# Kernel tuning notes

Measured on AMD Instinct MI355X. Metric: run time of the kernel, lower is better.

Reference implementation:

```python
import jax, jax.numpy as jnp
import numpy as np

DG, UF, Z, FD = 32, 4, 16, 16      # decoder grid, upsample factor, z bins, feat dim
H = W = DG * UF                     # 128 BEV resolution
S = 128                             # depth samples per ray
MLP_H = 32
X_MIN, X_MAX = -51.2, 51.2
Y_MIN, Y_MAX = -51.2, 51.2
Z_MIN, Z_MAX = -5.0, 3.0
D_MIN, D_MAX = 1.0, 50.0


def setup_inputs() -> dict:
    key = jax.random.key(0)
    ks = jax.random.split(key, 8)
    B, R, D = 2, 8192, 512
    out_dim = UF * UF * Z * FD
    s1 = 1.0 / np.sqrt(D); s2 = 1.0 / np.sqrt(FD); s3 = 1.0 / np.sqrt(MLP_H)
    return {
        'decoder_output': jax.random.normal(ks[0], (B, DG * DG, D), jnp.float32),
        'ray_origins': jax.random.normal(ks[1], (B, R, 3), jnp.float32),
        'ray_directions': jax.random.normal(ks[2], (B, R, 3), jnp.float32),
        'ln_g': jnp.ones((D,), jnp.float32),
        'ln_b': jnp.zeros((D,), jnp.float32),
        'W1': jax.random.uniform(ks[3], (D, out_dim), jnp.float32, -s1, s1),
        'b1': jnp.zeros((out_dim,), jnp.float32),
        'W2': jax.random.uniform(ks[4], (FD, MLP_H), jnp.float32, -s2, s2),
        'b2': jnp.zeros((MLP_H,), jnp.float32),
        'W3': jax.random.uniform(ks[5], (MLP_H, 1), jnp.float32, -s3, s3),
        'b3': jnp.zeros((1,), jnp.float32),
    }


def _build_nfg(dec, ln_g, ln_b, W1, b1):
    B = dec.shape[0]
    mu = dec.mean(-1, keepdims=True)
    var = dec.var(-1, keepdims=True)  # biased, matches torch LayerNorm
    x = (dec - mu) / jnp.sqrt(var + 1e-5) * ln_g + ln_b
    x = x @ W1 + b1
    x = x.reshape(B, DG, DG, UF, UF, Z, FD).transpose(0, 1, 3, 2, 4, 5, 6)
    x = x.reshape(B, H, W, Z, FD)
    return x.transpose(0, 4, 3, 1, 2)  # (B, F, Z, H, W)


def _trilinear_one(nfg_b, cw, ch, cd):
    # nfg_b: (F, Z, H, W); cw/ch/cd: (P,) in [-1,1] indexing W/H/Z resp.
    # align_corners=True mapping, zeros padding (mask OOB corners).
    fw = (cw + 1.0) * 0.5 * (W - 1)
    fh = (ch + 1.0) * 0.5 * (H - 1)
    fd = (cd + 1.0) * 0.5 * (Z - 1)
    w0 = jnp.floor(fw); h0 = jnp.floor(fh); d0 = jnp.floor(fd)
    tw = fw - w0; th = fh - h0; td = fd - d0
    out = jnp.zeros((nfg_b.shape[0], cw.shape[0]), nfg_b.dtype)
    for dd in (0, 1):
        for hh in (0, 1):
            for ww in (0, 1):
                di = d0 + dd; hi = h0 + hh; wi = w0 + ww
                wt = ((td if dd else 1.0 - td) * (th if hh else 1.0 - th)
                      * (tw if ww else 1.0 - tw))
                valid = ((di >= 0) & (di <= Z - 1) & (hi >= 0) & (hi <= H - 1)
                         & (wi >= 0) & (wi <= W - 1))
                dic = jnp.clip(di, 0, Z - 1).astype(jnp.int32)
                hic = jnp.clip(hi, 0, H - 1).astype(jnp.int32)
                wic = jnp.clip(wi, 0, W - 1).astype(jnp.int32)
                out = out + nfg_b[:, dic, hic, wic] * (wt * valid)
    return out  # (F, P)


def reference(decoder_output, ray_origins, ray_directions,
              ln_g, ln_b, W1, b1, W2, b2, W3, b3):
    nfg = _build_nfg(decoder_output, ln_g, ln_b, W1, b1)  # (B,F,Z,H,W)
    B, R, _ = ray_origins.shape
    t = jnp.linspace(0.0, 1.0, S, dtype=jnp.float32)
    depths = D_MIN + (D_MAX - D_MIN) * t                       # (S,)
    pts = ray_origins[:, :, None, :] + ray_directions[:, :, None, :] * depths[None, None, :, None]
    xn = 2.0 * (pts[..., 0] - X_MIN) / (X_MAX - X_MIN) - 1.0
    yn = 2.0 * (pts[..., 1] - Y_MIN) / (Y_MAX - Y_MIN) - 1.0
    zn = 2.0 * (pts[..., 2] - Z_MIN) / (Z_MAX - Z_MIN) - 1.0
    # torch grid_sample grid last dim = (x,y,z) -> (W,H,D); grid was stacked [y,x,z]
    cw = yn.reshape(B, -1); ch = xn.reshape(B, -1); cd = zn.reshape(B, -1)
    feats = jax.vmap(_trilinear_one)(nfg, cw, ch, cd)          # (B, F, R*S)
    feats = feats.transpose(0, 2, 1).reshape(B, R, S, FD)
    h = jax.nn.relu(feats @ W2 + b2)
    alpha = jax.nn.sigmoid((h @ W3 + b3)[..., 0])              # (B, R, S)
    oma = 1.0 - alpha + 1e-10
    trans = jnp.cumprod(
        jnp.concatenate([jnp.ones((B, R, 1), alpha.dtype), oma[..., :-1]], -1), -1)
    weights = alpha * trans
    pred_depths = (weights * depths[None, None, :]).sum(-1)    # (B, R)
    return pred_depths, weights, nfg
```

## Files before the change

### kernel.cpp

```cpp
#include <hip/hip_runtime.h>
#include <math.h>

#define DG   32
#define UF   4
#define ZB   16
#define FD   16
#define HH   128
#define WWID 128
#define SNUM 128
#define BATCH 2
#define RAYS  8192
#define NTOK  2048
#define DINP  512
#define ODIM  4096
#define MLPH  32

#define OUT_PRED_OFF 0
#define OUT_W_OFF    (BATCH*RAYS)
#define OUT_NFG_OFF  (OUT_W_OFF + BATCH*RAYS*SNUM)

typedef _Float16 half8 __attribute__((ext_vector_type(8)));
typedef _Float16 half4 __attribute__((ext_vector_type(4)));
typedef _Float16 h2 __attribute__((ext_vector_type(2)));
typedef float f32x4 __attribute__((ext_vector_type(4)));

#define GLDS16(gp, lp) \
    __builtin_amdgcn_global_load_lds((const __attribute__((address_space(1))) void*)(gp), \
                                     (__attribute__((address_space(3))) void*)(lp), 16, 0, 0)

__global__ __launch_bounds__(256) void ln_kernel(const float* __restrict__ dec,
                                                 const float* __restrict__ lng,
                                                 const float* __restrict__ lnb,
                                                 const float* __restrict__ W2,
                                                 const float* __restrict__ b2,
                                                 const float* __restrict__ W3,
                                                 _Float16* __restrict__ Af,
                                                 _Float16* __restrict__ W2f,
                                                 float* __restrict__ b2f,
                                                 float* __restrict__ w3f) {
    int t = blockIdx.x;
    int tid = threadIdx.x;
    const float2* row = reinterpret_cast<const float2*>(dec + (size_t)t * DINP);
    float2 v = row[tid];

    __shared__ float red[4];
    __shared__ float stat[2];

    float s = v.x + v.y;
    #pragma unroll
    for (int o = 32; o > 0; o >>= 1) s += __shfl_down(s, o);
    if ((tid & 63) == 0) red[tid >> 6] = s;
    __syncthreads();
    if (tid == 0) stat[0] = (red[0] + red[1] + red[2] + red[3]) * (1.0f / DINP);
    __syncthreads();
    float mu = stat[0];

    float dx = v.x - mu, dy = v.y - mu;
    float q = dx * dx + dy * dy;
    #pragma unroll
    for (int o = 32; o > 0; o >>= 1) q += __shfl_down(q, o);
    if ((tid & 63) == 0) red[tid >> 6] = q;
    __syncthreads();
    if (tid == 0) {
        float var = (red[0] + red[1] + red[2] + red[3]) * (1.0f / DINP);
        stat[1] = 1.0f / sqrtf(var + 1e-5f);
    }
    __syncthreads();
    float rstd = stat[1];

    int c = 2 * tid;
    h2 o2;
    o2.x = (_Float16)(dx * rstd * lng[c]     + lnb[c]);
    o2.y = (_Float16)(dy * rstd * lng[c + 1] + lnb[c + 1]);
    *reinterpret_cast<h2*>(Af + (size_t)t * DINP + c) = o2;

    if (blockIdx.x == 0 && tid < 128) {
        int jt = tid >> 6, l = tid & 63;
        int sub = l & 15, g = l >> 4;
        #pragma unroll
        for (int e = 0; e < 4; ++e) {
            W2f[(jt * 64 + l) * 4 + e] = (_Float16)W2[(g * 4 + e) * MLPH + jt * 16 + sub];
            b2f[(jt * 64 + l) * 4 + e] = b2[jt * 16 + g * 4 + e];
            w3f[(jt * 64 + l) * 4 + e] = W3[jt * 16 + g * 4 + e];
        }
    }
}

__global__ __launch_bounds__(256) void w1prep_kernel(const float* __restrict__ W1,
                                                     _Float16* __restrict__ W1T) {
    __shared__ float st[64][65];
    int c0 = blockIdx.x * 64;
    int k0 = blockIdx.y * 64;
    int tid = threadIdx.x;
    {
        int r = tid >> 2, cq = (tid & 3) * 16;
        const float* src = W1 + (size_t)(k0 + r) * ODIM + c0 + cq;
        #pragma unroll
        for (int q = 0; q < 4; ++q) {
            float4 v = *reinterpret_cast<const float4*>(src + q * 4);
            st[r][cq + q * 4 + 0] = v.x;
            st[r][cq + q * 4 + 1] = v.y;
            st[r][cq + q * 4 + 2] = v.z;
            st[r][cq + q * 4 + 3] = v.w;
        }
    }
    __syncthreads();
    {
        int cc = tid >> 2, kq = (tid & 3) * 16;
        _Float16 tmp[16];
        #pragma unroll
        for (int i = 0; i < 16; ++i) tmp[i] = (_Float16)st[kq + i][cc];
        _Float16* dst = W1T + (size_t)(c0 + cc) * DINP + k0 + kq;
        *reinterpret_cast<half8*>(dst)     = *reinterpret_cast<half8*>(&tmp[0]);
        *reinterpret_cast<half8*>(dst + 8) = *reinterpret_cast<half8*>(&tmp[8]);
    }
}

__global__ __launch_bounds__(256, 2) void gemm_mfma_kernel(
        const _Float16* __restrict__ Af, const _Float16* __restrict__ W1T,
        const float* __restrict__ bias, _Float16* __restrict__ gh) {
    __shared__ _Float16 As[128 * 32];
    __shared__ _Float16 Bs[128 * 32];

    int tid = threadIdx.x;
    int l = tid & 63, w = tid >> 6;
    int wr = w >> 1, wc = w & 1;
    int row0 = blockIdx.y * 128;
    int col0 = blockIdx.x * 128;

    const char* Ag0 = (const char*)Af + (size_t)(row0 + w * 32 + (l >> 2)) * (DINP * 2) + (l & 3) * 16;
    const char* Ag1 = Ag0 + 16 * (DINP * 2);
    const char* Bg0 = (const char*)W1T + (size_t)(col0 + w * 32 + (l >> 2)) * (DINP * 2) + (l & 3) * 16;
    const char* Bg1 = Bg0 + 16 * (DINP * 2);
    char* lA0 = (char*)As + w * 2048;
    char* lA1 = lA0 + 1024;
    char* lB0 = (char*)Bs + w * 2048;
    char* lB1 = lB0 + 1024;

    f32x4 acc[4][4] = {};

    for (int kk = 0; kk < DINP; kk += 32) {
        GLDS16(Ag0, lA0); GLDS16(Ag1, lA1);
        GLDS16(Bg0, lB0); GLDS16(Bg1, lB1);
        Ag0 += 64; Ag1 += 64; Bg0 += 64; Bg1 += 64;
        __syncthreads();

        half8 af[4], bf[4];
        #pragma unroll
        for (int m = 0; m < 4; ++m)
            af[m] = *reinterpret_cast<const half8*>(As + (wr * 64 + m * 16 + (l & 15)) * 32 + (l >> 4) * 8);
        #pragma unroll
        for (int n = 0; n < 4; ++n)
            bf[n] = *reinterpret_cast<const half8*>(Bs + (wc * 64 + n * 16 + (l & 15)) * 32 + (l >> 4) * 8);
        #pragma unroll
        for (int m = 0; m < 4; ++m)
            #pragma unroll
            for (int n = 0; n < 4; ++n)
                acc[m][n] = __builtin_amdgcn_mfma_f32_16x16x32_f16(af[m], bf[n], acc[m][n], 0, 0, 0);
        __syncthreads();
    }

    #pragma unroll
    for (int n = 0; n < 4; ++n) {
        int c = col0 + wc * 64 + n * 16 + (l & 15);
        float bv = bias[c];
        int f = c & 15, z = (c >> 4) & 15, v = (c >> 8) & 3, u = (c >> 10) & 3;
        #pragma unroll
        for (int m = 0; m < 4; ++m) {
            int rbase = row0 + wr * 64 + m * 16 + ((l >> 4) << 2);
            #pragma unroll
            for (int j = 0; j < 4; ++j) {
                int t = rbase + j;
                int bb = t >> 10;
                int g = t & 1023;
                int i = g >> 5, j2 = g & 31;
                int h = i * 4 + u, wq = j2 * 4 + v;
                size_t gaddr = ((((size_t)(bb * ZB + z) * HH + h) * WWID + wq) << 4) + f;
                gh[gaddr] = (_Float16)(acc[m][n][j] + bv);
            }
        }
    }
}

__global__ __launch_bounds__(256) void tp_kernel(const _Float16* __restrict__ gh,
                                                 float* __restrict__ nfg) {
    int blk = blockIdx.x;
    int bb = blk >> 11, z = (blk >> 7) & 15, h = blk & 127;
    __shared__ float sl[128 * 17];
    int tid = threadIdx.x;
    const uint4* src = reinterpret_cast<const uint4*>(gh + (size_t)blk * 2048);
    uint4 v = src[tid];
    int wv = tid >> 1, fb = (tid & 1) * 8;
    h2 p0 = __builtin_bit_cast(h2, v.x);
    h2 p1 = __builtin_bit_cast(h2, v.y);
    h2 p2 = __builtin_bit_cast(h2, v.z);
    h2 p3 = __builtin_bit_cast(h2, v.w);
    float* sr = &sl[wv * 17 + fb];
    sr[0] = (float)p0.x; sr[1] = (float)p0.y;
    sr[2] = (float)p1.x; sr[3] = (float)p1.y;
    sr[4] = (float)p2.x; sr[5] = (float)p2.y;
    sr[6] = (float)p3.x; sr[7] = (float)p3.y;
    __syncthreads();
    int f = tid >> 4, w0 = (tid & 15) * 8;
    float* dst = nfg + (((size_t)(bb * FD + f) * ZB + z) * (HH * WWID)) + h * WWID + w0;
    float4 o0, o1;
    o0.x = sl[(w0 + 0) * 17 + f]; o0.y = sl[(w0 + 1) * 17 + f];
    o0.z = sl[(w0 + 2) * 17 + f]; o0.w = sl[(w0 + 3) * 17 + f];
    o1.x = sl[(w0 + 4) * 17 + f]; o1.y = sl[(w0 + 5) * 17 + f];
    o1.z = sl[(w0 + 6) * 17 + f]; o1.w = sl[(w0 + 7) * 17 + f];
    *reinterpret_cast<float4*>(dst) = o0;
    *reinterpret_cast<float4*>(dst + 4) = o1;
}

__device__ __forceinline__ void gather_feat(const _Float16* __restrict__ gb,
                                            float px, float py, float pz,
                                            h2* __restrict__ a) {
    float fw = (py * (1.0f / 51.2f) + 1.0f) * 63.5f;
    float fh = (px * (1.0f / 51.2f) + 1.0f) * 63.5f;
    float fd = (pz + 5.0f) * (0.25f * 7.5f);
    float w0f = floorf(fw), h0f = floorf(fh), d0f = floorf(fd);
    float tw = fw - w0f, th = fh - h0f, td = fd - d0f;
    int w0 = (int)w0f, h0 = (int)h0f, d0 = (int)d0f;

    float aw0 = (w0 >= 0 && w0 <= WWID - 1) ? (1.0f - tw) : 0.0f;
    float aw1 = (w0 + 1 >= 0 && w0 + 1 <= WWID - 1) ? tw : 0.0f;
    float ah0 = (h0 >= 0 && h0 <= HH - 1) ? (1.0f - th) : 0.0f;
    float ah1 = (h0 + 1 >= 0 && h0 + 1 <= HH - 1) ? th : 0.0f;
    float ad0 = (d0 >= 0 && d0 <= ZB - 1) ? (1.0f - td) : 0.0f;
    float ad1 = (d0 + 1 >= 0 && d0 + 1 <= ZB - 1) ? td : 0.0f;

    if ((ad0 + ad1) * (ah0 + ah1) * (aw0 + aw1) <= 0.0f) return;

    int w0c = min(max(w0, 0), WWID - 1), w1c = min(max(w0 + 1, 0), WWID - 1);
    int h0c = min(max(h0, 0), HH - 1),   h1c = min(max(h0 + 1, 0), HH - 1);
    int d0c = min(max(d0, 0), ZB - 1),   d1c = min(max(d0 + 1, 0), ZB - 1);

    int od0 = d0c * (HH * WWID * FD), od1 = d1c * (HH * WWID * FD);
    int oh0 = h0c * (WWID * FD),      oh1 = h1c * (WWID * FD);
    int ow0 = w0c * FD,               ow1 = w1c * FD;

#define CORNER(OFF, WF) do { \
        const uint4* cp_ = reinterpret_cast<const uint4*>(gb + (OFF)); \
        uint4 A_ = cp_[0], B_ = cp_[1]; \
        _Float16 wh_ = (_Float16)(WF); \
        h2 w2_ = {wh_, wh_}; \
        a[0] += __builtin_bit_cast(h2, A_.x) * w2_; \
        a[1] += __builtin_bit_cast(h2, A_.y) * w2_; \
        a[2] += __builtin_bit_cast(h2, A_.z) * w2_; \
        a[3] += __builtin_bit_cast(h2, A_.w) * w2_; \
        a[4] += __builtin_bit_cast(h2, B_.x) * w2_; \
        a[5] += __builtin_bit_cast(h2, B_.y) * w2_; \
        a[6] += __builtin_bit_cast(h2, B_.z) * w2_; \
        a[7] += __builtin_bit_cast(h2, B_.w) * w2_; \
    } while (0)

    CORNER(od0 + oh0 + ow0, ad0 * ah0 * aw0);
    CORNER(od0 + oh0 + ow1, ad0 * ah0 * aw1);
    CORNER(od0 + oh1 + ow0, ad0 * ah1 * aw0);
    CORNER(od0 + oh1 + ow1, ad0 * ah1 * aw1);
    CORNER(od1 + oh0 + ow0, ad1 * ah0 * aw0);
    CORNER(od1 + oh0 + ow1, ad1 * ah0 * aw1);
    CORNER(od1 + oh1 + ow0, ad1 * ah1 * aw0);
    CORNER(od1 + oh1 + ow1, ad1 * ah1 * aw1);
#undef CORNER
}

#define SF 24
__global__ __launch_bounds__(256) void ray_fused_kernel(
        const float* __restrict__ orig, const float* __restrict__ dirs,
        const _Float16* __restrict__ gh,
        const _Float16* __restrict__ W2f, const float* __restrict__ b2f,
        const float* __restrict__ w3f, const float* __restrict__ b3,
        float* __restrict__ pred_out, float* __restrict__ w_out) {
    int tid = threadIdx.x;
    int lane = tid & 63, wvid = tid >> 6;
    int ray = blockIdx.x * 4 + wvid;
    int bb = ray >> 13;

    __shared__ _Float16 featLDS[4 * 128 * SF];
    _Float16* FL = &featLDS[wvid * 128 * SF];

    const float* o3 = orig + (size_t)ray * 3;
    const float* d3 = dirs + (size_t)ray * 3;
    float ox = o3[0], oy = o3[1], oz = o3[2];
    float dx = d3[0], dy = d3[1], dz = d3[2];

    const _Float16* gb = gh + (size_t)bb * (ZB * HH * WWID * FD);

    float t0 = 1.0f + 49.0f * ((float)lane * (1.0f / 127.0f));
    float t1 = 1.0f + 49.0f * ((float)(lane + 64) * (1.0f / 127.0f));

    h2 acc0[8] = {}, acc1[8] = {};
    gather_feat(gb, ox + dx * t0, oy + dy * t0, oz + dz * t0, acc0);
    gather_feat(gb, ox + dx * t1, oy + dy * t1, oz + dz * t1, acc1);

    {
        uint4 p0, p1;
        p0.x = __builtin_bit_cast(unsigned int, acc0[0]);
        p0.y = __builtin_bit_cast(unsigned int, acc0[1]);
        p0.z = __builtin_bit_cast(unsigned int, acc0[2]);
        p0.w = __builtin_bit_cast(unsigned int, acc0[3]);
        p1.x = __builtin_bit_cast(unsigned int, acc0[4]);
        p1.y = __builtin_bit_cast(unsigned int, acc0[5]);
        p1.z = __builtin_bit_cast(unsigned int, acc0[6]);
        p1.w = __builtin_bit_cast(unsigned int, acc0[7]);
        *reinterpret_cast<uint4*>(FL + lane * SF)     = p0;
        *reinterpret_cast<uint4*>(FL + lane * SF + 8) = p1;
        uint4 q0, q1;
        q0.x = __builtin_bit_cast(unsigned int, acc1[0]);
        q0.y = __builtin_bit_cast(unsigned int, acc1[1]);
        q0.z = __builtin_bit_cast(unsigned int, acc1[2]);
        q0.w = __builtin_bit_cast(unsigned int, acc1[3]);
        q1.x = __builtin_bit_cast(unsigned int, acc1[4]);
        q1.y = __builtin_bit_cast(unsigned int, acc1[5]);
        q1.z = __builtin_bit_cast(unsigned int, acc1[6]);
        q1.w = __builtin_bit_cast(unsigned int, acc1[7]);
        *reinterpret_cast<uint4*>(FL + (lane + 64) * SF)     = q0;
        *reinterpret_cast<uint4*>(FL + (lane + 64) * SF + 8) = q1;
    }

    half4 Af0 = *reinterpret_cast<const half4*>(W2f + lane * 4);
    half4 Af1 = *reinterpret_cast<const half4*>(W2f + (64 + lane) * 4);
    f32x4 b20 = *reinterpret_cast<const f32x4*>(b2f + lane * 4);
    f32x4 b21 = *reinterpret_cast<const f32x4*>(b2f + (64 + lane) * 4);
    f32x4 w30 = *reinterpret_cast<const f32x4*>(w3f + lane * 4);
    f32x4 w31 = *reinterpret_cast<const f32x4*>(w3f + (64 + lane) * 4);
    float b3v = b3[0];

    float at[8];
    #pragma unroll
    for (int tt = 0; tt < 8; ++tt) {
        half4 bfrag = *reinterpret_cast<const half4*>(
            FL + (tt * 16 + (lane & 15)) * SF + (lane >> 4) * 4);
        f32x4 c0 = __builtin_amdgcn_mfma_f32_16x16x16f16(Af0, bfrag, b20, 0, 0, 0);
        f32x4 c1 = __builtin_amdgcn_mfma_f32_16x16x16f16(Af1, bfrag, b21, 0, 0, 0);
        float p = 0.0f;
        #pragma unroll
        for (int r = 0; r < 4; ++r) {
            p = fmaf(fmaxf(c0[r], 0.0f), w30[r], p);
            p = fmaf(fmaxf(c1[r], 0.0f), w31[r], p);
        }
        p += __shfl_xor(p, 16);
        p += __shfl_xor(p, 32);
        at[tt] = p;
    }
    int g2 = lane >> 4;
    float aS0 = at[0];
    aS0 = (g2 == 1) ? at[1] : aS0;
    aS0 = (g2 == 2) ? at[2] : aS0;
    aS0 = (g2 == 3) ? at[3] : aS0;
    float aS1 = at[4];
    aS1 = (g2 == 1) ? at[5] : aS1;
    aS1 = (g2 == 2) ? at[6] : aS1;
    aS1 = (g2 == 3) ? at[7] : aS1;
    aS0 += b3v; aS1 += b3v;

    float alpha0 = 1.0f / (1.0f + __expf(-aS0));
    float alpha1 = 1.0f / (1.0f + __expf(-aS1));
    float oma0 = 1.0f - alpha0 + 1e-10f;
    float oma1 = 1.0f - alpha1 + 1e-10f;

    float P = oma0;
    #pragma unroll
    for (int off = 1; off < 64; off <<= 1) {
        float u = __shfl_up(P, off);
        if (lane >= off) P *= u;
    }
    float T64 = __shfl(P, 63);
    float Q = oma1;
    #pragma unroll
    for (int off = 1; off < 64; off <<= 1) {
        float u = __shfl_up(Q, off);
        if (lane >= off) Q *= u;
    }
    float e0 = __shfl_up(P, 1);
    if (lane == 0) e0 = 1.0f;
    float e1 = __shfl_up(Q, 1);
    e1 = (lane == 0) ? T64 : e1 * T64;

    float w0 = alpha0 * e0;
    float w1 = alpha1 * e1;
    w_out[(size_t)ray * SNUM + lane] = w0;
    w_out[(size_t)ray * SNUM + 64 + lane] = w1;

    float pv = w0 * t0 + w1 * t1;
    #pragma unroll
    for (int o = 32; o > 0; o >>= 1) pv += __shfl_xor(pv, o);
    if (lane == 0) pred_out[ray] = pv;
}

extern "C" void kernel_launch(void* const* d_in, const int* in_sizes, int n_in,
                              void* d_out, int out_size, void* d_ws, size_t ws_size,
                              hipStream_t stream) {
    const float* dec = (const float*)d_in[0];
    const float* ro  = (const float*)d_in[1];
    const float* rd  = (const float*)d_in[2];
    const float* lng = (const float*)d_in[3];
    const float* lnb = (const float*)d_in[4];
    const float* W1  = (const float*)d_in[5];
    const float* b1  = (const float*)d_in[6];
    const float* W2  = (const float*)d_in[7];
    const float* b2  = (const float*)d_in[8];
    const float* W3  = (const float*)d_in[9];
    const float* b3  = (const float*)d_in[10];

    float* out = (float*)d_out;
    char*  wsb = (char*)d_ws;
    _Float16* Af  = (_Float16*)wsb;
    _Float16* W1T = (_Float16*)(wsb + (2u << 20));
    _Float16* gh  = (_Float16*)(wsb + (6u << 20));
    _Float16* W2f = (_Float16*)(wsb + (23u << 20));
    float*    b2f = (float*)(wsb + (23u << 20) + 4096);
    float*    w3f = (float*)(wsb + (23u << 20) + 8192);

    ln_kernel<<<NTOK, 256, 0, stream>>>(dec, lng, lnb, W2, b2, W3, Af, W2f, b2f, w3f);

    dim3 pg(ODIM / 64, DINP / 64);
    w1prep_kernel<<<pg, 256, 0, stream>>>(W1, W1T);

    dim3 gg(ODIM / 128, NTOK / 128);
    gemm_mfma_kernel<<<gg, 256, 0, stream>>>(Af, W1T, b1, gh);

    tp_kernel<<<BATCH * ZB * HH, 256, 0, stream>>>(gh, out + OUT_NFG_OFF);

    ray_fused_kernel<<<BATCH * RAYS / 4, 256, 0, stream>>>(ro, rd, gh, W2f, b2f, w3f, b3,
                                                           out + OUT_PRED_OFF, out + OUT_W_OFF);
}
```

Measured before the change: 67.72 us.

## Merge independent kernels into shared launches to cut launch count

Merges the layernorm and W1 transpose kernels into one prep launch, with blocks split by index. It also merges the nfg transpose and the ray render kernel into one launch, interleaving even blocks (rays) and odd blocks (transpose). The goal is to remove two kernel launch gaps and let independent work overlap on the GPU. In exchange, both paths share one shared-memory allocation sized for the larger, which may lower occupancy. Register pressure is also set by the heavier path.

Result: slower. 71.85 us (+6.1%).

```diff
diff --git a/kernel.cpp b/kernel.cpp
--- a/kernel.cpp
+++ b/kernel.cpp
@@ -28,91 +28,92 @@
     __builtin_amdgcn_global_load_lds((const __attribute__((address_space(1))) void*)(gp), \
                                      (__attribute__((address_space(3))) void*)(lp), 16, 0, 0)
 
-__global__ __launch_bounds__(256) void ln_kernel(const float* __restrict__ dec,
-                                                 const float* __restrict__ lng,
-                                                 const float* __restrict__ lnb,
-                                                 const float* __restrict__ W2,
-                                                 const float* __restrict__ b2,
-                                                 const float* __restrict__ W3,
-                                                 _Float16* __restrict__ Af,
-                                                 _Float16* __restrict__ W2f,
-                                                 float* __restrict__ b2f,
-                                                 float* __restrict__ w3f) {
-    int t = blockIdx.x;
+__global__ __launch_bounds__(256) void prep_kernel(const float* __restrict__ dec,
+                                                   const float* __restrict__ lng,
+                                                   const float* __restrict__ lnb,
+                                                   const float* __restrict__ W2,
+                                                   const float* __restrict__ b2,
+                                                   const float* __restrict__ W3,
+                                                   const float* __restrict__ W1,
+                                                   _Float16* __restrict__ Af,
+                                                   _Float16* __restrict__ W1T,
+                                                   _Float16* __restrict__ W2f,
+                                                   float* __restrict__ b2f,
+                                                   float* __restrict__ w3f) {
     int tid = threadIdx.x;
-    const float2* row = reinterpret_cast<const float2*>(dec + (size_t)t * DINP);
-    float2 v = row[tid];
-
-    __shared__ float red[4];
-    __shared__ float stat[2];
-
-    float s = v.x + v.y;
-    #pragma unroll
-    for (int o = 32; o > 0; o >>= 1) s += __shfl_down(s, o);
-    if ((tid & 63) == 0) red[tid >> 6] = s;
-    __syncthreads();
-    if (tid == 0) stat[0] = (red[0] + red[1] + red[2] + red[3]) * (1.0f / DINP);
-    __syncthreads();
-    float mu = stat[0];
-
-    float dx = v.x - mu, dy = v.y - mu;
-    float q = dx * dx + dy * dy;
-    #pragma unroll
-    for (int o = 32; o > 0; o >>= 1) q += __shfl_down(q, o);
-    if ((tid & 63) == 0) red[tid >> 6] = q;
-    __syncthreads();
-    if (tid == 0) {
-        float var = (red[0] + red[1] + red[2] + red[3]) * (1.0f / DINP);
-        stat[1] = 1.0f / sqrtf(var + 1e-5f);
-    }
-    __syncthreads();
-    float rstd = stat[1];
-
-    int c = 2 * tid;
-    h2 o2;
-    o2.x = (_Float16)(dx * rstd * lng[c]     + lnb[c]);
-    o2.y = (_Float16)(dy * rstd * lng[c + 1] + lnb[c + 1]);
-    *reinterpret_cast<h2*>(Af + (size_t)t * DINP + c) = o2;
-
-    if (blockIdx.x == 0 && tid < 128) {
-        int jt = tid >> 6, l = tid & 63;
-        int sub = l & 15, g = l >> 4;
-        #pragma unroll
-        for (int e = 0; e < 4; ++e) {
-            W2f[(jt * 64 + l) * 4 + e] = (_Float16)W2[(g * 4 + e) * MLPH + jt * 16 + sub];
-            b2f[(jt * 64 + l) * 4 + e] = b2[jt * 16 + g * 4 + e];
-            w3f[(jt * 64 + l) * 4 + e] = W3[jt * 16 + g * 4 + e];
-        }
-    }
-}
-
-__global__ __launch_bounds__(256) void w1prep_kernel(const float* __restrict__ W1,
-                                                     _Float16* __restrict__ W1T) {
-    __shared__ float st[64][65];
-    int c0 = blockIdx.x * 64;
-    int k0 = blockIdx.y * 64;
-    int tid = threadIdx.x;
-    {
-        int r = tid >> 2, cq = (tid & 3) * 16;
-        const float* src = W1 + (size_t)(k0 + r) * ODIM + c0 + cq;
-        #pragma unroll
-        for (int q = 0; q < 4; ++q) {
-            float4 v = *reinterpret_cast<const float4*>(src + q * 4);
-            st[r][cq + q * 4 + 0] = v.x;
-            st[r][cq + q * 4 + 1] = v.y;
-            st[r][cq + q * 4 + 2] = v.z;
-            st[r][cq + q * 4 + 3] = v.w;
-        }
-    }
-    __syncthreads();
-    {
-        int cc = tid >> 2, kq = (tid & 3) * 16;
-        _Float16 tmp[16];
-        #pragma unroll
-        for (int i = 0; i < 16; ++i) tmp[i] = (_Float16)st[kq + i][cc];
-        _Float16* dst = W1T + (size_t)(c0 + cc) * DINP + k0 + kq;
-        *reinterpret_cast<half8*>(dst)     = *reinterpret_cast<half8*>(&tmp[0]);
-        *reinterpret_cast<half8*>(dst + 8) = *reinterpret_cast<half8*>(&tmp[8]);
+    if (blockIdx.x < NTOK) {
+        int t = blockIdx.x;
+        const float2* row = reinterpret_cast<const float2*>(dec + (size_t)t * DINP);
+        float2 v = row[tid];
+
+        __shared__ float red[4];
+        __shared__ float stat[2];
+
+        float s = v.x + v.y;
+        #pragma unroll
+        for (int o = 32; o > 0; o >>= 1) s += __shfl_down(s, o);
+        if ((tid & 63) == 0) red[tid >> 6] = s;
+        __syncthreads();
+        if (tid == 0) stat[0] = (red[0] + red[1] + red[2] + red[3]) * (1.0f / DINP);
+        __syncthreads();
+        float mu = stat[0];
+
+        float dx = v.x - mu, dy = v.y - mu;
+        float q = dx * dx + dy * dy;
+        #pragma unroll
+        for (int o = 32; o > 0; o >>= 1) q += __shfl_down(q, o);
+        if ((tid & 63) == 0) red[tid >> 6] = q;
+        __syncthreads();
+        if (tid == 0) {
+            float var = (red[0] + red[1] + red[2] + red[3]) * (1.0f / DINP);
+            stat[1] = 1.0f / sqrtf(var + 1e-5f);
+        }
+        __syncthreads();
+        float rstd = stat[1];
+
+        int c = 2 * tid;
+        h2 o2;
+        o2.x = (_Float16)(dx * rstd * lng[c]     + lnb[c]);
+        o2.y = (_Float16)(dy * rstd * lng[c + 1] + lnb[c + 1]);
+        *reinterpret_cast<h2*>(Af + (size_t)t * DINP + c) = o2;
+
+        if (blockIdx.x == 0 && tid < 128) {
+            int jt = tid >> 6, l = tid & 63;
+            int sub = l & 15, g = l >> 4;
+            #pragma unroll
+            for (int e = 0; e < 4; ++e) {
+                W2f[(jt * 64 + l) * 4 + e] = (_Float16)W2[(g * 4 + e) * MLPH + jt * 16 + sub];
+                b2f[(jt * 64 + l) * 4 + e] = b2[jt * 16 + g * 4 + e];
+                w3f[(jt * 64 + l) * 4 + e] = W3[jt * 16 + g * 4 + e];
+            }
+        }
+    } else {
+        __shared__ float st[64][65];
+        int blk = blockIdx.x - NTOK;
+        int c0 = (blk & 63) * 64;
+        int k0 = (blk >> 6) * 64;
+        {
+            int r = tid >> 2, cq = (tid & 3) * 16;
+            const float* src = W1 + (size_t)(k0 + r) * ODIM + c0 + cq;
+            #pragma unroll
+            for (int qq = 0; qq < 4; ++qq) {
+                float4 v = *reinterpret_cast<const float4*>(src + qq * 4);
+                st[r][cq + qq * 4 + 0] = v.x;
+                st[r][cq + qq * 4 + 1] = v.y;
+                st[r][cq + qq * 4 + 2] = v.z;
+                st[r][cq + qq * 4 + 3] = v.w;
+            }
+        }
+        __syncthreads();
+        {
+            int cc = tid >> 2, kq = (tid & 3) * 16;
+            _Float16 tmp[16];
+            #pragma unroll
+            for (int i = 0; i < 16; ++i) tmp[i] = (_Float16)st[kq + i][cc];
+            _Float16* dst = W1T + (size_t)(c0 + cc) * DINP + k0 + kq;
+            *reinterpret_cast<half8*>(dst)     = *reinterpret_cast<half8*>(&tmp[0]);
+            *reinterpret_cast<half8*>(dst + 8) = *reinterpret_cast<half8*>(&tmp[8]);
+        }
     }
 }
 
@@ -180,36 +181,6 @@
             }
         }
     }
-}
-
-__global__ __launch_bounds__(256) void tp_kernel(const _Float16* __restrict__ gh,
-                                                 float* __restrict__ nfg) {
-    int blk = blockIdx.x;
-    int bb = blk >> 11, z = (blk >> 7) & 15, h = blk & 127;
-    __shared__ float sl[128 * 17];
-    int tid = threadIdx.x;
-    const uint4* src = reinterpret_cast<const uint4*>(gh + (size_t)blk * 2048);
-    uint4 v = src[tid];
-    int wv = tid >> 1, fb = (tid & 1) * 8;
-    h2 p0 = __builtin_bit_cast(h2, v.x);
-    h2 p1 = __builtin_bit_cast(h2, v.y);
-    h2 p2 = __builtin_bit_cast(h2, v.z);
-    h2 p3 = __builtin_bit_cast(h2, v.w);
-    float* sr = &sl[wv * 17 + fb];
-    sr[0] = (float)p0.x; sr[1] = (float)p0.y;
-    sr[2] = (float)p1.x; sr[3] = (float)p1.y;
-    sr[4] = (float)p2.x; sr[5] = (float)p2.y;
-    sr[6] = (float)p3.x; sr[7] = (float)p3.y;
-    __syncthreads();
-    int f = tid >> 4, w0 = (tid & 15) * 8;
-    float* dst = nfg + (((size_t)(bb * FD + f) * ZB + z) * (HH * WWID)) + h * WWID + w0;
-    float4 o0, o1;
-    o0.x = sl[(w0 + 0) * 17 + f]; o0.y = sl[(w0 + 1) * 17 + f];
-    o0.z = sl[(w0 + 2) * 17 + f]; o0.w = sl[(w0 + 3) * 17 + f];
-    o1.x = sl[(w0 + 4) * 17 + f]; o1.y = sl[(w0 + 5) * 17 + f];
-    o1.z = sl[(w0 + 6) * 17 + f]; o1.w = sl[(w0 + 7) * 17 + f];
-    *reinterpret_cast<float4*>(dst) = o0;
-    *reinterpret_cast<float4*>(dst + 4) = o1;
 }
 
 __device__ __forceinline__ void gather_feat(const _Float16* __restrict__ gb,
@@ -266,127 +237,160 @@
 }
 
 #define SF 24
-__global__ __launch_bounds__(256) void ray_fused_kernel(
+#define RAYBLK (BATCH * RAYS / 4)
+__global__ __launch_bounds__(256) void consume_kernel(
         const float* __restrict__ orig, const float* __restrict__ dirs,
         const _Float16* __restrict__ gh,
         const _Float16* __restrict__ W2f, const float* __restrict__ b2f,
         const float* __restrict__ w3f, const float* __restrict__ b3,
-        float* __restrict__ pred_out, float* __restrict__ w_out) {
+        float* __restrict__ pred_out, float* __restrict__ w_out,
+        float* __restrict__ nfg) {
+    __shared__ __align__(16) char smem[4 * 128 * SF * 2];
     int tid = threadIdx.x;
-    int lane = tid & 63, wvid = tid >> 6;
-    int ray = blockIdx.x * 4 + wvid;
-    int bb = ray >> 13;
-
-    __shared__ _Float16 featLDS[4 * 128 * SF];
-    _Float16* FL = &featLDS[wvid * 128 * SF];
-
-    const float* o3 = orig + (size_t)ray * 3;
-    const float* d3 = dirs + (size_t)ray * 3;
-    float ox = o3[0], oy = o3[1], oz = o3[2];
-    float dx = d3[0], dy = d3[1], dz = d3[2];
-
-    const _Float16* gb = gh + (size_t)bb * (ZB * HH * WWID * FD);
-
-    float t0 = 1.0f + 49.0f * ((float)lane * (1.0f / 127.0f));
-    float t1 = 1.0f + 49.0f * ((float)(lane + 64) * (1.0f / 127.0f));
-
-    h2 acc0[8] = {}, acc1[8] = {};
-    gather_feat(gb, ox + dx * t0, oy + dy * t0, oz + dz * t0, acc0);
-    gather_feat(gb, ox + dx * t1, oy + dy * t1, oz + dz * t1, acc1);
-
-    {
-        uint4 p0, p1;
-        p0.x = __builtin_bit_cast(unsigned int, acc0[0]);
-        p0.y = __builtin_bit_cast(unsigned int, acc0[1]);
-        p0.z = __builtin_bit_cast(unsigned int, acc0[2]);
-        p0.w = __builtin_bit_cast(unsigned int, acc0[3]);
-        p1.x = __builtin_bit_cast(unsigned int, acc0[4]);
-        p1.y = __builtin_bit_cast(unsigned int, acc0[5]);
-        p1.z = __builtin_bit_cast(unsigned int, acc0[6]);
-        p1.w = __builtin_bit_cast(unsigned int, acc0[7]);
-        *reinterpret_cast<uint4*>(FL + lane * SF)     = p0;
-        *reinterpret_cast<uint4*>(FL + lane * SF + 8) = p1;
-        uint4 q0, q1;
-        q0.x = __builtin_bit_cast(unsigned int, acc1[0]);
-        q0.y = __builtin_bit_cast(unsigned int, acc1[1]);
-        q0.z = __builtin_bit_cast(unsigned int, acc1[2]);
-        q0.w = __builtin_bit_cast(unsigned int, acc1[3]);
-        q1.x = __builtin_bit_cast(unsigned int, acc1[4]);
-        q1.y = __builtin_bit_cast(unsigned int, acc1[5]);
-        q1.z = __builtin_bit_cast(unsigned int, acc1[6]);
-        q1.w = __builtin_bit_cast(unsigned int, acc1[7]);
-        *reinterpret_cast<uint4*>(FL + (lane + 64) * SF)     = q0;
-        *reinterpret_cast<uint4*>(FL + (lane + 64) * SF + 8) = q1;
+    int bx = blockIdx.x;
+
+    if ((bx & 1) == 0) {
+        _Float16* featLDS = reinterpret_cast<_Float16*>(smem);
+        int lane = tid & 63, wvid = tid >> 6;
+        int ray = (bx >> 1) * 4 + wvid;
+        int bb = ray >> 13;
+
+        _Float16* FL = &featLDS[wvid * 128 * SF];
+
+        const float* o3 = orig + (size_t)ray * 3;
+        const float* d3 = dirs + (size_t)ray * 3;
+        float ox = o3[0], oy = o3[1], oz = o3[2];
+        float dx = d3[0], dy = d3[1], dz = d3[2];
+
+        const _Float16* gb = gh + (size_t)bb * (ZB * HH * WWID * FD);
+
+        float t0 = 1.0f + 49.0f * ((float)lane * (1.0f / 127.0f));
+        float t1 = 1.0f + 49.0f * ((float)(lane + 64) * (1.0f / 127.0f));
+
+        h2 acc0[8] = {}, acc1[8] = {};
+        gather_feat(gb, ox + dx * t0, oy + dy * t0, oz + dz * t0, acc0);
+        gather_feat(gb, ox + dx * t1, oy + dy * t1, oz + dz * t1, acc1);
+
+        {
+            uint4 p0, p1;
+            p0.x = __builtin_bit_cast(unsigned int, acc0[0]);
+            p0.y = __builtin_bit_cast(unsigned int, acc0[1]);
+            p0.z = __builtin_bit_cast(unsigned int, acc0[2]);
+            p0.w = __builtin_bit_cast(unsigned int, acc0[3]);
+            p1.x = __builtin_bit_cast(unsigned int, acc0[4]);
+            p1.y = __builtin_bit_cast(unsigned int, acc0[5]);
+            p1.z = __builtin_bit_cast(unsigned int, acc0[6]);
+            p1.w = __builtin_bit_cast(unsigned int, acc0[7]);
+            *reinterpret_cast<uint4*>(FL + lane * SF)     = p0;
+            *reinterpret_cast<uint4*>(FL + lane * SF + 8) = p1;
+            uint4 q0, q1;
+            q0.x = __builtin_bit_cast(unsigned int, acc1[0]);
+            q0.y = __builtin_bit_cast(unsigned int, acc1[1]);
+            q0.z = __builtin_bit_cast(unsigned int, acc1[2]);
+            q0.w = __builtin_bit_cast(unsigned int, acc1[3]);
+            q1.x = __builtin_bit_cast(unsigned int, acc1[4]);
+            q1.y = __builtin_bit_cast(unsigned int, acc1[5]);
+            q1.z = __builtin_bit_cast(unsigned int, acc1[6]);
+            q1.w = __builtin_bit_cast(unsigned int, acc1[7]);
+            *reinterpret_cast<uint4*>(FL + (lane + 64) * SF)     = q0;
+            *reinterpret_cast<uint4*>(FL + (lane + 64) * SF + 8) = q1;
+        }
+
+        half4 Af0 = *reinterpret_cast<const half4*>(W2f + lane * 4);
+        half4 Af1 = *reinterpret_cast<const half4*>(W2f + (64 + lane) * 4);
+        f32x4 b20 = *reinterpret_cast<const f32x4*>(b2f + lane * 4);
+        f32x4 b21 = *reinterpret_cast<const f32x4*>(b2f + (64 + lane) * 4);
+        f32x4 w30 = *reinterpret_cast<const f32x4*>(w3f + lane * 4);
+        f32x4 w31 = *reinterpret_cast<const f32x4*>(w3f + (64 + lane) * 4);
+        float b3v = b3[0];
+
+        float at[8];
+        #pragma unroll
+        for (int tt = 0; tt < 8; ++tt) {
+            half4 bfrag = *reinterpret_cast<const half4*>(
+                FL + (tt * 16 + (lane & 15)) * SF + (lane >> 4) * 4);
+            f32x4 c0 = __builtin_amdgcn_mfma_f32_16x16x16f16(Af0, bfrag, b20, 0, 0, 0);
+            f32x4 c1 = __builtin_amdgcn_mfma_f32_16x16x16f16(Af1, bfrag, b21, 0, 0, 0);
+            float p = 0.0f;
+            #pragma unroll
+            for (int r = 0; r < 4; ++r) {
+                p = fmaf(fmaxf(c0[r], 0.0f), w30[r], p);
+                p = fmaf(fmaxf(c1[r], 0.0f), w31[r], p);
+            }
+            p += __shfl_xor(p, 16);
+            p += __shfl_xor(p, 32);
+            at[tt] = p;
+        }
+        int g2 = lane >> 4;
+        float aS0 = at[0];
+        aS0 = (g2 == 1) ? at[1] : aS0;
+        aS0 = (g2 == 2) ? at[2] : aS0;
+        aS0 = (g2 == 3) ? at[3] : aS0;
+        float aS1 = at[4];
+        aS1 = (g2 == 1) ? at[5] : aS1;
+        aS1 = (g2 == 2) ? at[6] : aS1;
+        aS1 = (g2 == 3) ? at[7] : aS1;
+        aS0 += b3v; aS1 += b3v;
+
+        float alpha0 = 1.0f / (1.0f + __expf(-aS0));
+        float alpha1 = 1.0f / (1.0f + __expf(-aS1));
+        float oma0 = 1.0f - alpha0 + 1e-10f;
+        float oma1 = 1.0f - alpha1 + 1e-10f;
+
+        float P = oma0;
+        #pragma unroll
+        for (int off = 1; off < 64; off <<= 1) {
+            float u = __shfl_up(P, off);
+            if (lane >= off) P *= u;
+        }
+        float T64 = __shfl(P, 63);
+        float Q = oma1;
+        #pragma unroll
+        for (int off = 1; off < 64; off <<= 1) {
+            float u = __shfl_up(Q, off);
+            if (lane >= off) Q *= u;
+        }
+        float e0 = __shfl_up(P, 1);
+        if (lane == 0) e0 = 1.0f;
+        float e1 = __shfl_up(Q, 1);
+        e1 = (lane == 0) ? T64 : e1 * T64;
+
+        float w0 = alpha0 * e0;
+        float w1 = alpha1 * e1;
+        w_out[(size_t)ray * SNUM + lane] = w0;
+        w_out[(size_t)ray * SNUM + 64 + lane] = w1;
+
+        float pv = w0 * t0 + w1 * t1;
+        #pragma unroll
+        for (int o = 32; o > 0; o >>= 1) pv += __shfl_xor(pv, o);
+        if (lane == 0) pred_out[ray] = pv;
+    } else {
+        float* sl = reinterpret_cast<float*>(smem);
+        int blk = bx >> 1;
+        int bb = blk >> 11, z = (blk >> 7) & 15, h = blk & 127;
+        const uint4* src = reinterpret_cast<const uint4*>(gh + (size_t)blk * 2048);
+        uint4 v = src[tid];
+        int wv = tid >> 1, fb = (tid & 1) * 8;
+        h2 p0 = __builtin_bit_cast(h2, v.x);
+        h2 p1 = __builtin_bit_cast(h2, v.y);
+        h2 p2 = __builtin_bit_cast(h2, v.z);
+        h2 p3 = __builtin_bit_cast(h2, v.w);
+        float* sr = &sl[wv * 17 + fb];
+        sr[0] = (float)p0.x; sr[1] = (float)p0.y;
+        sr[2] = (float)p1.x; sr[3] = (float)p1.y;
+        sr[4] = (float)p2.x; sr[5] = (float)p2.y;
+        sr[6] = (float)p3.x; sr[7] = (float)p3.y;
+        __syncthreads();
+        int f = tid >> 4, w0 = (tid & 15) * 8;
+        float* dst = nfg + (((size_t)(bb * FD + f) * ZB + z) * (HH * WWID)) + h * WWID + w0;
+        float4 o0, o1;
+        o0.x = sl[(w0 + 0) * 17 + f]; o0.y = sl[(w0 + 1) * 17 + f];
+        o0.z = sl[(w0 + 2) * 17 + f]; o0.w = sl[(w0 + 3) * 17 + f];
+        o1.x = sl[(w0 + 4) * 17 + f]; o1.y = sl[(w0 + 5) * 17 + f];
+        o1.z = sl[(w0 + 6) * 17 + f]; o1.w = sl[(w0 + 7) * 17 + f];
+        *reinterpret_cast<float4*>(dst) = o0;
+        *reinterpret_cast<float4*>(dst + 4) = o1;
     }
-
-    half4 Af0 = *reinterpret_cast<const half4*>(W2f + lane * 4);
-    half4 Af1 = *reinterpret_cast<const half4*>(W2f + (64 + lane) * 4);
-    f32x4 b20 = *reinterpret_cast<const f32x4*>(b2f + lane * 4);
-    f32x4 b21 = *reinterpret_cast<const f32x4*>(b2f + (64 + lane) * 4);
-    f32x4 w30 = *reinterpret_cast<const f32x4*>(w3f + lane * 4);
-    f32x4 w31 = *reinterpret_cast<const f32x4*>(w3f + (64 + lane) * 4);
-    float b3v = b3[0];
-
-    float at[8];
-    #pragma unroll
-    for (int tt = 0; tt < 8; ++tt) {
-        half4 bfrag = *reinterpret_cast<const half4*>(
-            FL + (tt * 16 + (lane & 15)) * SF + (lane >> 4) * 4);
-        f32x4 c0 = __builtin_amdgcn_mfma_f32_16x16x16f16(Af0, bfrag, b20, 0, 0, 0);
-        f32x4 c1 = __builtin_amdgcn_mfma_f32_16x16x16f16(Af1, bfrag, b21, 0, 0, 0);
-        float p = 0.0f;
-        #pragma unroll
-        for (int r = 0; r < 4; ++r) {
-            p = fmaf(fmaxf(c0[r], 0.0f), w30[r], p);
-            p = fmaf(fmaxf(c1[r], 0.0f), w31[r], p);
-        }
-        p += __shfl_xor(p, 16);
-        p += __shfl_xor(p, 32);
-        at[tt] = p;
-    }
-    int g2 = lane >> 4;
-    float aS0 = at[0];
-    aS0 = (g2 == 1) ? at[1] : aS0;
-    aS0 = (g2 == 2) ? at[2] : aS0;
-    aS0 = (g2 == 3) ? at[3] : aS0;
-    float aS1 = at[4];
-    aS1 = (g2 == 1) ? at[5] : aS1;
-    aS1 = (g2 == 2) ? at[6] : aS1;
-    aS1 = (g2 == 3) ? at[7] : aS1;
-    aS0 += b3v; aS1 += b3v;
-
-    float alpha0 = 1.0f / (1.0f + __expf(-aS0));
-    float alpha1 = 1.0f / (1.0f + __expf(-aS1));
-    float oma0 = 1.0f - alpha0 + 1e-10f;
-    float oma1 = 1.0f - alpha1 + 1e-10f;
-
-    float P = oma0;
-    #pragma unroll
-    for (int off = 1; off < 64; off <<= 1) {
-        float u = __shfl_up(P, off);
-        if (lane >= off) P *= u;
-    }
-    float T64 = __shfl(P, 63);
-    float Q = oma1;
-    #pragma unroll
-    for (int off = 1; off < 64; off <<= 1) {
-        float u = __shfl_up(Q, off);
-        if (lane >= off) Q *= u;
-    }
-    float e0 = __shfl_up(P, 1);
-    if (lane == 0) e0 = 1.0f;
-    float e1 = __shfl_up(Q, 1);
-    e1 = (lane == 0) ? T64 : e1 * T64;
-
-    float w0 = alpha0 * e0;
-    float w1 = alpha1 * e1;
-    w_out[(size_t)ray * SNUM + lane] = w0;
-    w_out[(size_t)ray * SNUM + 64 + lane] = w1;
-
-    float pv = w0 * t0 + w1 * t1;
-    #pragma unroll
-    for (int o = 32; o > 0; o >>= 1) pv += __shfl_xor(pv, o);
-    if (lane == 0) pred_out[ray] = pv;
 }
 
 extern "C" void kernel_launch(void* const* d_in, const int* in_sizes, int n_in,
@@ -413,16 +417,13 @@
     float*    b2f = (float*)(wsb + (23u << 20) + 4096);
     float*    w3f = (float*)(wsb + (23u << 20) + 8192);
 
-    ln_kernel<<<NTOK, 256, 0, stream>>>(dec, lng, lnb, W2, b2, W3, Af, W2f, b2f, w3f);
-
-    dim3 pg(ODIM / 64, DINP / 64);
-    w1prep_kernel<<<pg, 256, 0, stream>>>(W1, W1T);
+    prep_kernel<<<NTOK + (ODIM / 64) * (DINP / 64), 256, 0, stream>>>(
+        dec, lng, lnb, W2, b2, W3, W1, Af, W1T, W2f, b2f, w3f);
 
     dim3 gg(ODIM / 128, NTOK / 128);
     gemm_mfma_kernel<<<gg, 256, 0, stream>>>(Af, W1T, b1, gh);
 
-    tp_kernel<<<BATCH * ZB * HH, 256, 0, stream>>>(gh, out + OUT_NFG_OFF);
-
-    ray_fused_kernel<<<BATCH * RAYS / 4, 256, 0, stream>>>(ro, rd, gh, W2f, b2f, w3f, b3,
-                                                           out + OUT_PRED_OFF, out + OUT_W_OFF);
+    consume_kernel<<<2 * RAYBLK, 256, 0, stream>>>(ro, rd, gh, W2f, b2f, w3f, b3,
+                                                   out + OUT_PRED_OFF, out + OUT_W_OFF,
+                                                   out + OUT_NFG_OFF);
 }
```
